# Kernel tuning notes

Hardware: AMD Instinct MI355X
Metric: run time of the kernel (lower is better)

## Reference

```python
import jax, jax.numpy as jnp
import numpy as np

# config constants
D = 1024       # main_dim
HD = 64        # attn_head_dim
NH = 16        # attention heads = D // HD
H = 16         # main_head_num (routing heads)
KH = 8         # main_key_head_num
KC = 2         # main_key_repeat_num (KH*KC == H)
N = 128        # block_size
E = 4096       # total_layer_expert_num
RE = 4         # aux_router_expert_num
DE = 4         # selected experts per router
ET = RE * DE   # 16
B, S = 1, 2048
T = B * S
BC = T // N    # 16
EPS = 1e-5
THETA = 10000.0


def rmsnorm(x, w):
    return x * jax.lax.rsqrt(jnp.mean(x * x, axis=-1, keepdims=True) + EPS) * w


def l2norm(x):
    n = jnp.sqrt(jnp.sum(x * x, axis=-1, keepdims=True))
    return x / jnp.maximum(n, EPS)


def rope(x):
    # x: (b, h, s, a); matches RotaryEmb: y1 = x1*cos + x2*sin, y2 = -x1*sin + x2*cos
    a = x.shape[-1]
    s = x.shape[2]
    inv_freq = (1.0 / THETA) ** (jnp.arange(0, a, 2, dtype=jnp.float32) / a)
    freqs = jnp.arange(s, dtype=jnp.float32)[:, None] * inv_freq[None, :]  # (s, a/2)
    cos, sin = jnp.cos(freqs), jnp.sin(freqs)
    x1, x2 = jnp.split(x, 2, axis=-1)
    return jnp.concatenate([x1 * cos + x2 * sin, -x1 * sin + x2 * cos], axis=-1)


def setup_inputs() -> dict:
    key = jax.random.key(0)
    ks = jax.random.split(key, 10)
    return {
        "x_input": jax.random.normal(ks[0], (B, S, D), jnp.float32),
        "indices": jax.random.randint(ks[1], (BC, RE, DE), 0, E),
        "scores": jax.random.normal(ks[2], (T, ET, H), jnp.float32),
        "attn_w": jax.random.normal(ks[3], (D, 3 * D), jnp.float32) * 0.02,
        "attn_out_w": jax.random.normal(ks[4], (D, D), jnp.float32) * 0.02,
        "attn_norm_w": jnp.ones((D,), jnp.float32),
        "ffn_norm_w": jnp.ones((D,), jnp.float32),
        "ffn_experts": jax.random.normal(ks[5], (3, E, D, 1), jnp.float32) * 0.02,
        "keys": jax.random.normal(ks[6], (KH, D, E), jnp.float32) * 0.02,
        "head_probs": jnp.full((1, RE, E, H), 1.0 / H, jnp.float32)
                      + 0.01 * jax.random.normal(ks[7], (1, RE, E, H), jnp.float32),
        "score_probs": jnp.full((2, 1, RE, E, H), 0.5, jnp.float32)
                       + 0.01 * jax.random.normal(ks[8], (2, 1, RE, E, H), jnp.float32),
    }


def reference(x_input, indices, scores, attn_w, attn_out_w, attn_norm_w,
              ffn_norm_w, ffn_experts, keys, head_probs, score_probs):
    # --- attention block ---
    x = rmsnorm(x_input, attn_norm_w)
    qkv = x @ attn_w                                   # (b, s, 3d)
    xq, xk, xv = jnp.split(qkv, 3, axis=-1)

    def heads(t):  # 'b s (h a) -> b h s a'
        return t.reshape(B, S, NH, HD).transpose(0, 2, 1, 3)

    xq, xk, xv = heads(xq), heads(xk), heads(xv)
    xq, xk = l2norm(xq), l2norm(xk)                    # qk_norm
    xq, xk = rope(xq), rope(xk)

    att = jnp.einsum('bhqa,bhka->bhqk', xq, xk) / np.sqrt(HD)
    causal = jnp.tril(jnp.ones((S, S), bool))
    att = jnp.where(causal, att, -jnp.inf)
    att = jax.nn.softmax(att, axis=-1)
    x_attn = jnp.einsum('bhqk,bhka->bhqa', att, xv)
    x_attn = x_attn.transpose(0, 2, 1, 3).reshape(B, S, D)
    x_attn_output = x_attn @ attn_out_w
    x_ffn_input = x_attn_output + x_input

    # --- product-key routing ---
    x_ffn = rmsnorm(x_ffn_input, ffn_norm_w)
    xf = x_ffn.reshape(T, D)

    keys_r = jnp.repeat(keys, KC, axis=0)              # (H, D, E)
    ms = jnp.einsum('td,hde->teh', xf, keys_r)         # (T, E, H)

    idx_flat = indices.reshape(BC, ET)                 # (BC, ET)
    idx_tok = jnp.repeat(idx_flat, N, axis=0)          # (T, ET), token t -> block t//N
    main_g = jnp.take_along_axis(ms, idx_tok[:, :, None], axis=1)  # (T, ET, H)

    r_idx = jnp.arange(RE)[None, :, None]
    sp = score_probs[:, 0]                             # (2, RE, E, H)
    sp_g = sp[:, r_idx, indices]                       # (2, BC, RE, DE, H)
    sp_g = jnp.repeat(sp_g.reshape(2, BC, ET, H), N, axis=1)       # (2, T, ET, H)

    comb = jax.nn.sigmoid(sp_g[0] * main_g + sp_g[1] * scores)     # (T, ET, H)

    hp_g = head_probs[0][r_idx, indices]               # (BC, RE, DE, H)
    hp_g = jnp.repeat(hp_g.reshape(BC, ET, H), N, axis=0)          # (T, ET, H)

    w = jnp.sum(comb * hp_g, axis=-1)                  # (T, ET) pair weights

    # --- grouped GEMM over tiny (d -> expert_dim -> d) experts, SwiGLU ---
    Wg = ffn_experts[:, idx_tok]                       # (3, T, ET, D, expert_dim)
    h0 = jnp.einsum('td,tedk->tek', xf, Wg[0])
    h1 = jnp.einsum('td,tedk->tek', xf, Wg[1])
    act = jax.nn.silu(h0) * h1 * w[:, :, None]         # (T, ET, expert_dim)
    out = jnp.einsum('tek,tedk->td', act, Wg[2])       # sum over selected experts

    return out.reshape(B, S, D) + x_ffn_input
```

## Files before the change

kernel.cpp:

```cpp
#include <hip/hip_runtime.h>
#include <hip/hip_bf16.h>
#include <math.h>

#define D_   1024
#define HD_  64
#define NH_  16
#define H_   16
#define KH_  8
#define NT_  128
#define E_   4096
#define RE_  4
#define DE_  4
#define ET_  16
#define S_   2048
#define T_   2048
#define BC_  16
#define EPS_ 1e-5f

typedef short s16x8 __attribute__((ext_vector_type(8)));
typedef float f32x4 __attribute__((ext_vector_type(4)));

__device__ __forceinline__ unsigned short f2bf(float f) {
    union { float f; unsigned int u; } v; v.f = f;
    unsigned int r = (v.u + 0x7fffu + ((v.u >> 16) & 1u)) >> 16;
    return (unsigned short)r;
}

#define GLOAD16(gp, lp) __builtin_amdgcn_global_load_lds(                      \
    (__attribute__((address_space(1))) void*)(gp),                             \
    (__attribute__((address_space(3))) void*)(lp), 16, 0, 0)

__global__ __launch_bounds__(256) void preprocess_kernel(
    const float* __restrict__ x, const float* __restrict__ attn_norm_w,
    unsigned short* __restrict__ xnb,
    const float* __restrict__ attn_w, unsigned short* __restrict__ wqkvT,
    const float* __restrict__ attn_out_w, unsigned short* __restrict__ woutT,
    const float* __restrict__ keys, const int* __restrict__ indices,
    unsigned short* __restrict__ kgath)
{
    __shared__ float tile[32][33];
    __shared__ float sred[4];
    int bid = blockIdx.x, tid = threadIdx.x;

    if (bid < 2048) {
        int row = bid;
        float4 v = ((const float4*)(x + (size_t)row * D_))[tid];
        float ss = v.x*v.x + v.y*v.y + v.z*v.z + v.w*v.w;
#pragma unroll
        for (int off = 32; off > 0; off >>= 1) ss += __shfl_xor(ss, off);
        if ((tid & 63) == 0) sred[tid >> 6] = ss;
        __syncthreads();
        float tot = sred[0] + sred[1] + sred[2] + sred[3];
        float scale = rsqrtf(tot * (1.0f / D_) + EPS_);
        float4 wv = ((const float4*)attn_norm_w)[tid];
        ushort4 o;
        o.x = f2bf(v.x * scale * wv.x);
        o.y = f2bf(v.y * scale * wv.y);
        o.z = f2bf(v.z * scale * wv.z);
        o.w = f2bf(v.w * scale * wv.w);
        *(ushort4*)(xnb + (size_t)row * D_ + tid * 4) = o;
    } else if (bid < 6144) {
        const float* src; unsigned short* dst; int R, Ncols, bx, by;
        if (bid < 5120) {
            int cid = bid - 2048;
            src = attn_w; dst = wqkvT; R = D_; Ncols = 3 * D_;
            bx = (cid % 96) * 32; by = (cid / 96) * 32;
        } else {
            int cid = bid - 5120;
            src = attn_out_w; dst = woutT; R = D_; Ncols = D_;
            bx = (cid & 31) * 32; by = (cid >> 5) * 32;
        }
        int tx = tid & 31, ty = tid >> 5;
#pragma unroll
        for (int rr = 0; rr < 32; rr += 8)
            tile[ty + rr][tx] = src[(size_t)(by + ty + rr) * Ncols + bx + tx];
        __syncthreads();
#pragma unroll
        for (int rr = 0; rr < 32; rr += 8)
            dst[(size_t)(bx + ty + rr) * R + by + tx] = f2bf(tile[tx][ty + rr]);
    } else {
        int gid = bid - 6144;
        int pair = gid >> 3, kh = gid & 7;
        int idx = indices[pair];
        const float* kp = keys + (size_t)kh * D_ * E_ + idx;
        int d = tid * 4;
        ushort4 o;
        o.x = f2bf(kp[(size_t)(d + 0) * E_]);
        o.y = f2bf(kp[(size_t)(d + 1) * E_]);
        o.z = f2bf(kp[(size_t)(d + 2) * E_]);
        o.w = f2bf(kp[(size_t)(d + 3) * E_]);
        *(ushort4*)(kgath + ((size_t)pair * KH_ + kh) * D_ + d) = o;
    }
}

__global__ __launch_bounds__(256) void rmsnorm_dual_kernel(
    const float* __restrict__ x, const float* __restrict__ w,
    float* __restrict__ out, unsigned short* __restrict__ outb)
{
    int row = blockIdx.x, tid = threadIdx.x;
    __shared__ float sred[4];
    float4 v = ((const float4*)(x + (size_t)row * D_))[tid];
    float ss = v.x*v.x + v.y*v.y + v.z*v.z + v.w*v.w;
#pragma unroll
    for (int off = 32; off > 0; off >>= 1) ss += __shfl_xor(ss, off);
    if ((tid & 63) == 0) sred[tid >> 6] = ss;
    __syncthreads();
    float tot = sred[0] + sred[1] + sred[2] + sred[3];
    float scale = rsqrtf(tot * (1.0f / D_) + EPS_);
    float4 wv = ((const float4*)w)[tid];
    float4 o;
    o.x = v.x * scale * wv.x;
    o.y = v.y * scale * wv.y;
    o.z = v.z * scale * wv.z;
    o.w = v.w * scale * wv.w;
    ((float4*)(out + (size_t)row * D_))[tid] = o;
    ushort4 ob;
    ob.x = f2bf(o.x); ob.y = f2bf(o.y); ob.z = f2bf(o.z); ob.w = f2bf(o.w);
    *(ushort4*)(outb + (size_t)row * D_ + tid * 4) = ob;
}

__global__ __launch_bounds__(256) void transpose_v_kernel(
    const unsigned short* __restrict__ src, unsigned short* __restrict__ dst)
{
    __shared__ unsigned short tile[32][34];
    int h  = blockIdx.z;
    int d0 = blockIdx.x * 32;
    int s0 = blockIdx.y * 32;
    int tx = threadIdx.x & 31, ty = threadIdx.x >> 5;
    const unsigned short* sp = src + ((size_t)h * S_ + s0) * HD_ + d0;
#pragma unroll
    for (int rr = 0; rr < 32; rr += 8)
        tile[ty + rr][tx] = sp[(size_t)(ty + rr) * HD_ + tx];
    __syncthreads();
    unsigned short* dp = dst + ((size_t)h * HD_ + d0) * S_ + s0;
#pragma unroll
    for (int rr = 0; rr < 32; rr += 8)
        dp[(size_t)(ty + rr) * S_ + tx] = tile[tx][ty + rr];
}

template <int WITH_RES>
__global__ __launch_bounds__(256) void mfma_gemm_kernel(
    const unsigned short* __restrict__ A, const unsigned short* __restrict__ Bt,
    const float* __restrict__ res, float* __restrict__ C,
    int M, int N, int K)
{
    __shared__ __align__(16) short As[128][32];
    __shared__ __align__(16) short Bs[128][32];
    int tid = threadIdx.x;
    int wave = tid >> 6, lane = tid & 63;
    int ml = lane & 15, q = lane >> 4;
    int wr = wave >> 1, wc = wave & 1;
    int bm = blockIdx.y * 128, bn = blockIdx.x * 128;
    int srow = tid >> 2;
    int scol = (tid & 3) * 8;

    f32x4 acc[4][4];
#pragma unroll
    for (int i = 0; i < 4; i++)
#pragma unroll
        for (int j = 0; j < 4; j++) acc[i][j] = (f32x4){0.f, 0.f, 0.f, 0.f};

    const unsigned short* Ap = A  + (size_t)(bm + srow) * K + scol;
    const unsigned short* Bp = Bt + (size_t)(bn + srow) * K + scol;
    short* ldsA0 = &As[wave * 16][0];
    short* ldsA1 = &As[64 + wave * 16][0];
    short* ldsB0 = &Bs[wave * 16][0];
    short* ldsB1 = &Bs[64 + wave * 16][0];

    for (int k0 = 0; k0 < K; k0 += 32) {
        __syncthreads();
        GLOAD16(Ap + k0, ldsA0);
        GLOAD16(Ap + (size_t)64 * K + k0, ldsA1);
        GLOAD16(Bp + k0, ldsB0);
        GLOAD16(Bp + (size_t)64 * K + k0, ldsB1);
        __syncthreads();

        s16x8 af[4], bf[4];
#pragma unroll
        for (int i = 0; i < 4; i++)
            af[i] = *(const s16x8*)(&As[wr * 64 + i * 16 + ml][q * 8]);
#pragma unroll
        for (int j = 0; j < 4; j++)
            bf[j] = *(const s16x8*)(&Bs[wc * 64 + j * 16 + ml][q * 8]);
#pragma unroll
        for (int i = 0; i < 4; i++)
#pragma unroll
            for (int j = 0; j < 4; j++)
                acc[i][j] = __builtin_amdgcn_mfma_f32_16x16x32_bf16(
                    af[i], bf[j], acc[i][j], 0, 0, 0);
    }

#pragma unroll
    for (int i = 0; i < 4; i++) {
#pragma unroll
        for (int j = 0; j < 4; j++) {
            int col = bn + wc * 64 + j * 16 + ml;
#pragma unroll
            for (int r = 0; r < 4; r++) {
                int row = bm + wr * 64 + i * 16 + q * 4 + r;
                float v = acc[i][j][r];
                if (WITH_RES) v += res[(size_t)row * N + col];
                C[(size_t)row * N + col] = v;
            }
        }
    }
}

__global__ __launch_bounds__(256) void mfma_gemm_qkv_kernel(
    const unsigned short* __restrict__ A, const unsigned short* __restrict__ Bt,
    unsigned short* __restrict__ qh, unsigned short* __restrict__ khb,
    unsigned short* __restrict__ vhb)
{
    const int K = D_;
    __shared__ __align__(16) short As[128][32];
    __shared__ __align__(16) short Bs[128][32];
    int tid = threadIdx.x;
    int wave = tid >> 6, lane = tid & 63;
    int ml = lane & 15, q = lane >> 4;
    int wr = wave >> 1, wc = wave & 1;
    int bm = blockIdx.y * 128, bn = blockIdx.x * 128;
    int srow = tid >> 2;
    int scol = (tid & 3) * 8;

    f32x4 acc[4][4];
#pragma unroll
    for (int i = 0; i < 4; i++)
#pragma unroll
        for (int j = 0; j < 4; j++) acc[i][j] = (f32x4){0.f, 0.f, 0.f, 0.f};

    const unsigned short* Ap = A  + (size_t)(bm + srow) * K + scol;
    const unsigned short* Bp = Bt + (size_t)(bn + srow) * K + scol;
    short* ldsA0 = &As[wave * 16][0];
    short* ldsA1 = &As[64 + wave * 16][0];
    short* ldsB0 = &Bs[wave * 16][0];
    short* ldsB1 = &Bs[64 + wave * 16][0];

    for (int k0 = 0; k0 < K; k0 += 32) {
        __syncthreads();
        GLOAD16(Ap + k0, ldsA0);
        GLOAD16(Ap + (size_t)64 * K + k0, ldsA1);
        GLOAD16(Bp + k0, ldsB0);
        GLOAD16(Bp + (size_t)64 * K + k0, ldsB1);
        __syncthreads();

        s16x8 af[4], bf[4];
#pragma unroll
        for (int i = 0; i < 4; i++)
            af[i] = *(const s16x8*)(&As[wr * 64 + i * 16 + ml][q * 8]);
#pragma unroll
        for (int j = 0; j < 4; j++)
            bf[j] = *(const s16x8*)(&Bs[wc * 64 + j * 16 + ml][q * 8]);
#pragma unroll
        for (int i = 0; i < 4; i++)
#pragma unroll
            for (int j = 0; j < 4; j++)
                acc[i][j] = __builtin_amdgcn_mfma_f32_16x16x32_bf16(
                    af[i], bf[j], acc[i][j], 0, 0, 0);
    }

    int sel = blockIdx.x >> 3;
    int h = ((blockIdx.x & 7) << 1) + wc;
    unsigned short* dst = (sel == 0) ? qh : (sel == 1) ? khb : vhb;
    float qscale = (sel == 0) ? 0.125f : 1.0f;
    float if0 = exp2f((float)ml * (-13.287712379549449f / 32.0f));
    float if1 = exp2f((float)(16 + ml) * (-13.287712379549449f / 32.0f));

#pragma unroll
    for (int i = 0; i < 4; i++) {
#pragma unroll
        for (int r = 0; r < 4; r++) {
            int row = bm + wr * 64 + i * 16 + q * 4 + r;
            float v0 = acc[i][0][r], v1 = acc[i][1][r];
            float v2 = acc[i][2][r], v3 = acc[i][3][r];
            if (sel < 2) {
                float ss = v0*v0 + v1*v1 + v2*v2 + v3*v3;
#pragma unroll
                for (int off = 1; off < 16; off <<= 1)
                    ss += __shfl_xor(ss, off);
                float inv = qscale / fmaxf(sqrtf(ss), EPS_);
                v0 *= inv; v1 *= inv; v2 *= inv; v3 *= inv;
                float sn0, cs0, sn1, cs1;
                sincosf((float)row * if0, &sn0, &cs0);
                sincosf((float)row * if1, &sn1, &cs1);
                float o0 = v0 * cs0 + v2 * sn0;
                float o2 = v2 * cs0 - v0 * sn0;
                float o1 = v1 * cs1 + v3 * sn1;
                float o3 = v3 * cs1 - v1 * sn1;
                v0 = o0; v1 = o1; v2 = o2; v3 = o3;
            }
            size_t base = ((size_t)h * S_ + row) * HD_;
            dst[base +      ml] = f2bf(v0);
            dst[base + 16 + ml] = f2bf(v1);
            dst[base + 32 + ml] = f2bf(v2);
            dst[base + 48 + ml] = f2bf(v3);
        }
    }
}

#define FS 72
__global__ __launch_bounds__(256) void flash_attn_mfma_kernel(
    const unsigned short* __restrict__ qh, const unsigned short* __restrict__ khb,
    const unsigned short* __restrict__ vhT, unsigned short* __restrict__ aob)
{
    __shared__ __align__(16) short Ks[2][64][FS];
    __shared__ __align__(16) short Vs[2][64][FS];
    __shared__ __align__(16) short Ps[4][16][FS];
    int b = blockIdx.x;
    int xcd = b & 7, j = b >> 3;
    int h = 2 * xcd + (j & 1);
    int pp = (j >> 1) & 15;
    int t = (j >> 5) ? (31 - pp) : pp;
    int tid = threadIdx.x;
    int wq = tid >> 6;
    int lane = tid & 63;
    int ml = lane & 15, quad = lane >> 4;
    int srow = tid >> 2;
    int sc = (tid & 3) * 16;
    const unsigned short* Qb = qh  + (size_t)h * S_ * HD_;
    const unsigned short* Kb = khb + (size_t)h * S_ * HD_;
    const unsigned short* Vt = vhT + (size_t)h * HD_ * S_;

    int q0 = t * 64;
    int qrow = q0 + wq * 16 + ml;
    s16x8 aq0 = *(const s16x8*)(Qb + (size_t)qrow * HD_ + quad * 8);
    s16x8 aq1 = *(const s16x8*)(Qb + (size_t)qrow * HD_ + 32 + quad * 8);

    float ps[4];
    f32x4 o[4];
#pragma unroll
    for (int r = 0; r < 4; r++) ps[r] = 0.f;
#pragma unroll
    for (int nb = 0; nb < 4; nb++) o[nb] = (f32x4){0.f, 0.f, 0.f, 0.f};

    int4 kr0, kr1, vr0, vr1;
    {
        const unsigned short* kp = Kb + (size_t)srow * HD_ + sc;
        kr0 = *(const int4*)kp; kr1 = *(const int4*)(kp + 8);
        const unsigned short* vp = Vt + (size_t)srow * S_ + sc;
        vr0 = *(const int4*)vp; vr1 = *(const int4*)(vp + 8);
        *(int4*)(&Ks[0][srow][sc]) = kr0; *(int4*)(&Ks[0][srow][sc + 8]) = kr1;
        *(int4*)(&Vs[0][srow][sc]) = vr0; *(int4*)(&Vs[0][srow][sc + 8]) = vr1;
    }

    for (int kt = 0; kt <= t; kt++) {
        int k0 = kt * 64;
        int cur = kt & 1;
        if (kt < t) {
            const unsigned short* kp = Kb + (size_t)(k0 + 64 + srow) * HD_ + sc;
            kr0 = *(const int4*)kp; kr1 = *(const int4*)(kp + 8);
            const unsigned short* vp = Vt + (size_t)srow * S_ + k0 + 64 + sc;
            vr0 = *(const int4*)vp; vr1 = *(const int4*)(vp + 8);
        }
        __syncthreads();

        f32x4 s[4];
#pragma unroll
        for (int nb = 0; nb < 4; nb++) s[nb] = (f32x4){0.f, 0.f, 0.f, 0.f};
        __builtin_amdgcn_s_setprio(1);
#pragma unroll
        for (int nb = 0; nb < 4; nb++) {
            s16x8 b0 = *(const s16x8*)(&Ks[cur][nb * 16 + ml][quad * 8]);
            s16x8 b1 = *(const s16x8*)(&Ks[cur][nb * 16 + ml][32 + quad * 8]);
            s[nb] = __builtin_amdgcn_mfma_f32_16x16x32_bf16(aq0, b0, s[nb], 0, 0, 0);
            s[nb] = __builtin_amdgcn_mfma_f32_16x16x32_bf16(aq1, b1, s[nb], 0, 0, 0);
        }
        __builtin_amdgcn_s_setprio(0);

#pragma unroll
        for (int nb = 0; nb < 4; nb++)
#pragma unroll
            for (int r = 0; r < 4; r++) {
                float pe = __expf(s[nb][r]);
                if (kt == t && (nb * 16 + ml) > (wq * 16 + quad * 4 + r))
                    pe = 0.f;
                ps[r] += pe;
                Ps[wq][quad * 4 + r][nb * 16 + ml] = (short)f2bf(pe);
            }

        s16x8 ap0 = *(const s16x8*)(&Ps[wq][ml][quad * 8]);
        s16x8 ap1 = *(const s16x8*)(&Ps[wq][ml][32 + quad * 8]);
        __builtin_amdgcn_s_setprio(1);
#pragma unroll
        for (int nb = 0; nb < 4; nb++) {
            s16x8 b0 = *(const s16x8*)(&Vs[cur][nb * 16 + ml][quad * 8]);
            s16x8 b1 = *(const s16x8*)(&Vs[cur][nb * 16 + ml][32 + quad * 8]);
            o[nb] = __builtin_amdgcn_mfma_f32_16x16x32_bf16(ap0, b0, o[nb], 0, 0, 0);
            o[nb] = __builtin_amdgcn_mfma_f32_16x16x32_bf16(ap1, b1, o[nb], 0, 0, 0);
        }
        __builtin_amdgcn_s_setprio(0);

        if (kt < t) {
            *(int4*)(&Ks[cur ^ 1][srow][sc])     = kr0;
            *(int4*)(&Ks[cur ^ 1][srow][sc + 8]) = kr1;
            *(int4*)(&Vs[cur ^ 1][srow][sc])     = vr0;
            *(int4*)(&Vs[cur ^ 1][srow][sc + 8]) = vr1;
        }
    }

#pragma unroll
    for (int r = 0; r < 4; r++) {
        float l = ps[r];
#pragma unroll
        for (int off = 1; off < 16; off <<= 1)
            l += __shfl_xor(l, off);
        float inv = 1.0f / l;
        int row = q0 + wq * 16 + quad * 4 + r;
#pragma unroll
        for (int nb = 0; nb < 4; nb++)
            aob[(size_t)row * D_ + h * HD_ + nb * 16 + ml] =
                f2bf(o[nb][r] * inv);
    }
}

__global__ __launch_bounds__(256) void score_gemm_kernel(
    const unsigned short* __restrict__ xfb, const unsigned short* __restrict__ kgath,
    float* __restrict__ msbufp)
{
    __shared__ __align__(16) short As[128][32];
    __shared__ __align__(16) short Bs[128][32];
    int c  = blockIdx.x >> 3;
    int sk = blockIdx.x & 7;
    const unsigned short* A  = xfb   + (size_t)c * 128 * D_ + sk * 128;
    const unsigned short* Bt = kgath + (size_t)c * 128 * D_ + sk * 128;
    int tid = threadIdx.x;
    int wave = tid >> 6, lane = tid & 63;
    int ml = lane & 15, q = lane >> 4;
    int wr = wave >> 1, wc = wave & 1;
    int srow = tid >> 2;
    int scol = (tid & 3) * 8;

    f32x4 acc[4][4];
#pragma unroll
    for (int i = 0; i < 4; i++)
#pragma unroll
        for (int j = 0; j < 4; j++) acc[i][j] = (f32x4){0.f, 0.f, 0.f, 0.f};

    const unsigned short* Ap = A  + (size_t)srow * D_ + scol;
    const unsigned short* Bp = Bt + (size_t)srow * D_ + scol;
    short* ldsA0 = &As[wave * 16][0];
    short* ldsA1 = &As[64 + wave * 16][0];
    short* ldsB0 = &Bs[wave * 16][0];
    short* ldsB1 = &Bs[64 + wave * 16][0];

    for (int k0 = 0; k0 < 128; k0 += 32) {
        __syncthreads();
        GLOAD16(Ap + k0, ldsA0);
        GLOAD16(Ap + (size_t)64 * D_ + k0, ldsA1);
        GLOAD16(Bp + k0, ldsB0);
        GLOAD16(Bp + (size_t)64 * D_ + k0, ldsB1);
        __syncthreads();

        s16x8 af[4], bf[4];
#pragma unroll
        for (int i = 0; i < 4; i++)
            af[i] = *(const s16x8*)(&As[wr * 64 + i * 16 + ml][q * 8]);
#pragma unroll
        for (int j = 0; j < 4; j++)
            bf[j] = *(const s16x8*)(&Bs[wc * 64 + j * 16 + ml][q * 8]);
#pragma unroll
        for (int i = 0; i < 4; i++)
#pragma unroll
            for (int j = 0; j < 4; j++)
                acc[i][j] = __builtin_amdgcn_mfma_f32_16x16x32_bf16(
                    af[i], bf[j], acc[i][j], 0, 0, 0);
    }

    float* out = msbufp + (size_t)blockIdx.x * 128 * 128;
#pragma unroll
    for (int i = 0; i < 4; i++)
#pragma unroll
        for (int j = 0; j < 4; j++) {
            int col = wc * 64 + j * 16 + ml;
#pragma unroll
            for (int r = 0; r < 4; r++) {
                int row = wr * 64 + i * 16 + q * 4 + r;
                out[(size_t)row * 128 + col] = acc[i][j][r];
            }
        }
}

__global__ __launch_bounds__(256) void moe_kernel(
    const float* __restrict__ xf, const float* __restrict__ xfi,
    const int* __restrict__ indices, const float* __restrict__ msbufp,
    const float* __restrict__ scores,
    const float* __restrict__ score_probs, const float* __restrict__ head_probs,
    const float* __restrict__ experts, float* __restrict__ out)
{
    int g = blockIdx.x, tid = threadIdx.x;
    int c = g >> 5;
    int t0 = c * NT_ + (g & 31) * 4;
    __shared__ int sidx[ET_];
    __shared__ float sw[4][ET_];
    __shared__ float sact[4][ET_];
    __shared__ float sx[4][D_];
    if (tid < ET_) sidx[tid] = indices[c * ET_ + tid];
#pragma unroll
    for (int tt = 0; tt < 4; tt++)
        ((float4*)sx[tt])[tid] =
            ((const float4*)(xf + (size_t)(t0 + tt) * D_))[tid];
    {
        int e = tid >> 4, hh = tid & 15;
        int idxe = indices[c * ET_ + e];
        int rr = e >> 2;
        float sp0 = score_probs[((size_t)rr * E_ + idxe) * H_ + hh];
        float sp1 = score_probs[((size_t)(RE_ + rr) * E_ + idxe) * H_ + hh];
        float hp  = head_probs[((size_t)rr * E_ + idxe) * H_ + hh];
#pragma unroll
        for (int tt = 0; tt < 4; tt++) {
            int t = t0 + tt;
            int trow = t & 127;
            const float* mp = msbufp + ((size_t)(c * 8) * 128 + trow) * 128
                                     + e * 8 + (hh >> 1);
            float ms = 0.f;
#pragma unroll
            for (int sck = 0; sck < 8; sck++)
                ms += mp[(size_t)sck * 128 * 128];
            float scv = scores[(size_t)t * (ET_ * H_) + tid];
            float z = sp0 * ms + sp1 * scv;
            float term = hp / (1.0f + __expf(-z));
#pragma unroll
            for (int off = 1; off < 16; off <<= 1)
                term += __shfl_xor(term, off);
            if (hh == 0) sw[tt][e] = term;
        }
    }
    __syncthreads();

    int wv = tid >> 6, lane = tid & 63;
#pragma unroll
    for (int ee = 0; ee < 4; ee++) {
        int e = wv * 4 + ee;
        int idx = sidx[e];
        size_t base = (size_t)idx * D_;
        float p0[4] = {0.f, 0.f, 0.f, 0.f};
        float p1[4] = {0.f, 0.f, 0.f, 0.f};
#pragma unroll
        for (int rr = 0; rr < 4; rr++) {
            int dd = rr * 256 + lane * 4;
            float4 w0 = *(const float4*)(experts + base + dd);
            float4 w1 = *(const float4*)(experts + (size_t)E_ * D_ + base + dd);
#pragma unroll
            for (int tt = 0; tt < 4; tt++) {
                float4 xr = *(const float4*)(&sx[tt][dd]);
                p0[tt] += xr.x*w0.x + xr.y*w0.y + xr.z*w0.z + xr.w*w0.w;
                p1[tt] += xr.x*w1.x + xr.y*w1.y + xr.z*w1.z + xr.w*w1.w;
            }
        }
#pragma unroll
        for (int tt = 0; tt < 4; tt++) {
#pragma unroll
            for (int off = 32; off > 0; off >>= 1) {
                p0[tt] += __shfl_xor(p0[tt], off);
                p1[tt] += __shfl_xor(p1[tt], off);
            }
        }
        if (lane == 0) {
#pragma unroll
            for (int tt = 0; tt < 4; tt++)
                sact[tt][e] = p0[tt] / (1.0f + __expf(-p0[tt])) * p1[tt]
                              * sw[tt][e];
        }
    }
    __syncthreads();

    float4 a0 = {0,0,0,0}, a1 = {0,0,0,0}, a2 = {0,0,0,0}, a3 = {0,0,0,0};
    const float* w2base = experts + (size_t)2 * E_ * D_;
#pragma unroll
    for (int e = 0; e < ET_; e++) {
        float4 w2 = *(const float4*)(w2base + (size_t)sidx[e] * D_ + tid * 4);
        float c0 = sact[0][e], c1 = sact[1][e], c2 = sact[2][e], c3 = sact[3][e];
        a0.x += c0 * w2.x; a0.y += c0 * w2.y; a0.z += c0 * w2.z; a0.w += c0 * w2.w;
        a1.x += c1 * w2.x; a1.y += c1 * w2.y; a1.z += c1 * w2.z; a1.w += c1 * w2.w;
        a2.x += c2 * w2.x; a2.y += c2 * w2.y; a2.z += c2 * w2.z; a2.w += c2 * w2.w;
        a3.x += c3 * w2.x; a3.y += c3 * w2.y; a3.z += c3 * w2.z; a3.w += c3 * w2.w;
    }
#pragma unroll
    for (int tt = 0; tt < 4; tt++) {
        float4 av = (tt == 0) ? a0 : (tt == 1) ? a1 : (tt == 2) ? a2 : a3;
        size_t o = (size_t)(t0 + tt) * D_ + tid * 4;
        float4 rv = *(const float4*)(xfi + o);
        float4 ov;
        ov.x = av.x + rv.x;
        ov.y = av.y + rv.y;
        ov.z = av.z + rv.z;
        ov.w = av.w + rv.w;
        *(float4*)(out + o) = ov;
    }
}

extern "C" void kernel_launch(void* const* d_in, const int* in_sizes, int n_in,
                              void* d_out, int out_size, void* d_ws, size_t ws_size,
                              hipStream_t stream)
{
    (void)in_sizes; (void)n_in; (void)out_size; (void)ws_size;
    const float* x_input     = (const float*)d_in[0];
    const int*   indices     = (const int*)d_in[1];
    const float* scores      = (const float*)d_in[2];
    const float* attn_w      = (const float*)d_in[3];
    const float* attn_out_w  = (const float*)d_in[4];
    const float* attn_norm_w = (const float*)d_in[5];
    const float* ffn_norm_w  = (const float*)d_in[6];
    const float* ffn_experts = (const float*)d_in[7];
    const float* keys        = (const float*)d_in[8];
    const float* head_probs  = (const float*)d_in[9];
    const float* score_probs = (const float*)d_in[10];
    float* out = (float*)d_out;

    float* ws = (float*)d_ws;
    const size_t MF = 1024 * 1024;
    unsigned short* qh    = (unsigned short*)ws;
    unsigned short* khb   = (unsigned short*)(ws + 1 * MF);
    unsigned short* vhb   = (unsigned short*)(ws + 2 * MF);
    unsigned short* vhT   = (unsigned short*)(ws + 3 * MF);
    float* xfi            = ws + 4 * MF;
    unsigned short* xnb   = (unsigned short*)(ws + 6 * MF);
    unsigned short* aob   = (unsigned short*)(ws + 6 * MF);
    unsigned short* woutT = (unsigned short*)(ws + 7 * MF);
    unsigned short* wqkvT = (unsigned short*)(ws + 8 * MF);
    float* xf             = ws + 8 * MF;
    unsigned short* kgath = (unsigned short*)(ws + 10 * MF);
    unsigned short* xfb   = (unsigned short*)(ws + 11 * MF);
    float* msbufp         = ws + 12 * MF;

    preprocess_kernel<<<8192, 256, 0, stream>>>(
        x_input, attn_norm_w, xnb, attn_w, wqkvT, attn_out_w, woutT,
        keys, indices, kgath);

    {
        dim3 g(3 * D_ / 128, T_ / 128);
        mfma_gemm_qkv_kernel<<<g, 256, 0, stream>>>(xnb, wqkvT, qh, khb, vhb);
    }

    {
        dim3 g(HD_ / 32, S_ / 32, NH_);
        transpose_v_kernel<<<g, 256, 0, stream>>>(vhb, vhT);
    }

    flash_attn_mfma_kernel<<<(S_ / 64) * NH_, 256, 0, stream>>>(qh, khb, vhT, aob);

    {
        dim3 g(D_ / 128, T_ / 128);
        mfma_gemm_kernel<1><<<g, 256, 0, stream>>>(aob, woutT, x_input, xfi,
                                                   T_, D_, D_);
    }

    rmsnorm_dual_kernel<<<T_, 256, 0, stream>>>(xfi, ffn_norm_w, xf, xfb);

    score_gemm_kernel<<<BC_ * 8, 256, 0, stream>>>(xfb, kgath, msbufp);

    moe_kernel<<<T_ / 4, 256, 0, stream>>>(xf, xfi, indices, msbufp, scores,
                                           score_probs, head_probs,
                                           ffn_experts, out);
}
```

Before: 375.0 us.

## Gather keys via coalesced row reads and fuse V transpose into QKV epilogue

The key-column gather, which did strided reads with stride E per element, is replaced by blocks that each load a full contiguous keys row into shared memory and pick the 256 selected columns. A new tiled transpose kernel then reorders the result into the kgath layout. Separately, the QKV GEMM epilogue now writes V directly in transposed layout, so the standalone V transpose kernel is removed. The trade-off is that the whole keys tensor is now streamed (128 MB of coalesced reads) and V is written with strided stores, in exchange for avoiding uncoalesced gathers and one kernel launch.

```diff
diff --git a/kernel.cpp b/kernel.cpp
--- a/kernel.cpp
+++ b/kernel.cpp
@@ -36,10 +36,11 @@
     const float* __restrict__ attn_w, unsigned short* __restrict__ wqkvT,
     const float* __restrict__ attn_out_w, unsigned short* __restrict__ woutT,
     const float* __restrict__ keys, const int* __restrict__ indices,
-    unsigned short* __restrict__ kgath)
+    unsigned short* __restrict__ tmpT)
 {
     __shared__ float tile[32][33];
     __shared__ float sred[4];
+    __shared__ float rowbuf[E_];
     int bid = blockIdx.x, tid = threadIdx.x;
 
     if (bid < 2048) {
@@ -79,17 +80,37 @@
         for (int rr = 0; rr < 32; rr += 8)
             dst[(size_t)(bx + ty + rr) * R + by + tx] = f2bf(tile[tx][ty + rr]);
     } else {
-        int gid = bid - 6144;
-        int pair = gid >> 3, kh = gid & 7;
-        int idx = indices[pair];
-        const float* kp = keys + (size_t)kh * D_ * E_ + idx;
-        int d = tid * 4;
-        ushort4 o;
-        o.x = f2bf(kp[(size_t)(d + 0) * E_]);
-        o.y = f2bf(kp[(size_t)(d + 1) * E_]);
-        o.z = f2bf(kp[(size_t)(d + 2) * E_]);
-        o.w = f2bf(kp[(size_t)(d + 3) * E_]);
-        *(ushort4*)(kgath + ((size_t)pair * KH_ + kh) * D_ + d) = o;
+        int id = bid - 6144;
+        int kh = id >> 10;
+        int d  = id & (D_ - 1);
+        const float* rowp = keys + ((size_t)kh * D_ + d) * E_;
+#pragma unroll
+        for (int pass = 0; pass < 4; pass++)
+            ((float4*)rowbuf)[tid + pass * 256] =
+                ((const float4*)rowp)[tid + pass * 256];
+        __syncthreads();
+        int idx = indices[tid];
+        tmpT[((size_t)kh * D_ + d) * 256 + tid] = f2bf(rowbuf[idx]);
+    }
+}
+
+__global__ __launch_bounds__(256) void transpose_keys_kernel(
+    const unsigned short* __restrict__ tmpT, unsigned short* __restrict__ kgath)
+{
+    __shared__ unsigned short tile[32][34];
+    int p0 = blockIdx.x * 32;
+    int d0 = blockIdx.y * 32;
+    int kh = blockIdx.z;
+    int tx = threadIdx.x & 31, ty = threadIdx.x >> 5;
+#pragma unroll
+    for (int rr = 0; rr < 32; rr += 8)
+        tile[ty + rr][tx] = tmpT[((size_t)kh * D_ + d0 + ty + rr) * 256 + p0 + tx];
+    __syncthreads();
+#pragma unroll
+    for (int rr = 0; rr < 32; rr += 8) {
+        int p = p0 + ty + rr;
+        int n = (p >> 4) * 128 + (p & 15) * 8 + kh;
+        kgath[(size_t)n * D_ + d0 + tx] = tile[tx][ty + rr];
     }
 }
 
@@ -119,25 +140,6 @@
     *(ushort4*)(outb + (size_t)row * D_ + tid * 4) = ob;
 }
 
-__global__ __launch_bounds__(256) void transpose_v_kernel(
-    const unsigned short* __restrict__ src, unsigned short* __restrict__ dst)
-{
-    __shared__ unsigned short tile[32][34];
-    int h  = blockIdx.z;
-    int d0 = blockIdx.x * 32;
-    int s0 = blockIdx.y * 32;
-    int tx = threadIdx.x & 31, ty = threadIdx.x >> 5;
-    const unsigned short* sp = src + ((size_t)h * S_ + s0) * HD_ + d0;
-#pragma unroll
-    for (int rr = 0; rr < 32; rr += 8)
-        tile[ty + rr][tx] = sp[(size_t)(ty + rr) * HD_ + tx];
-    __syncthreads();
-    unsigned short* dp = dst + ((size_t)h * HD_ + d0) * S_ + s0;
-#pragma unroll
-    for (int rr = 0; rr < 32; rr += 8)
-        dp[(size_t)(ty + rr) * S_ + tx] = tile[tx][ty + rr];
-}
-
 template <int WITH_RES>
 __global__ __launch_bounds__(256) void mfma_gemm_kernel(
     const unsigned short* __restrict__ A, const unsigned short* __restrict__ Bt,
@@ -209,7 +211,7 @@
 __global__ __launch_bounds__(256) void mfma_gemm_qkv_kernel(
     const unsigned short* __restrict__ A, const unsigned short* __restrict__ Bt,
     unsigned short* __restrict__ qh, unsigned short* __restrict__ khb,
-    unsigned short* __restrict__ vhb)
+    unsigned short* __restrict__ vhT)
 {
     const int K = D_;
     __shared__ __align__(16) short As[128][32];
@@ -260,7 +262,6 @@
 
     int sel = blockIdx.x >> 3;
     int h = ((blockIdx.x & 7) << 1) + wc;
-    unsigned short* dst = (sel == 0) ? qh : (sel == 1) ? khb : vhb;
     float qscale = (sel == 0) ? 0.125f : 1.0f;
     float if0 = exp2f((float)ml * (-13.287712379549449f / 32.0f));
     float if1 = exp2f((float)(16 + ml) * (-13.287712379549449f / 32.0f));
@@ -287,12 +288,19 @@
                 float o1 = v1 * cs1 + v3 * sn1;
                 float o3 = v3 * cs1 - v1 * sn1;
                 v0 = o0; v1 = o1; v2 = o2; v3 = o3;
+                unsigned short* dst = (sel == 0) ? qh : khb;
+                size_t base = ((size_t)h * S_ + row) * HD_;
+                dst[base +      ml] = f2bf(v0);
+                dst[base + 16 + ml] = f2bf(v1);
+                dst[base + 32 + ml] = f2bf(v2);
+                dst[base + 48 + ml] = f2bf(v3);
+            } else {
+                size_t base = ((size_t)h * HD_ + ml) * S_ + row;
+                vhT[base            ] = f2bf(v0);
+                vhT[base + 16 * S_  ] = f2bf(v1);
+                vhT[base + 32 * S_  ] = f2bf(v2);
+                vhT[base + 48 * S_  ] = f2bf(v3);
             }
-            size_t base = ((size_t)h * S_ + row) * HD_;
-            dst[base +      ml] = f2bf(v0);
-            dst[base + 16 + ml] = f2bf(v1);
-            dst[base + 32 + ml] = f2bf(v2);
-            dst[base + 48 + ml] = f2bf(v3);
         }
     }
 }
@@ -610,7 +618,7 @@
     const size_t MF = 1024 * 1024;
     unsigned short* qh    = (unsigned short*)ws;
     unsigned short* khb   = (unsigned short*)(ws + 1 * MF);
-    unsigned short* vhb   = (unsigned short*)(ws + 2 * MF);
+    unsigned short* tmpT  = (unsigned short*)(ws + 2 * MF);
     unsigned short* vhT   = (unsigned short*)(ws + 3 * MF);
     float* xfi            = ws + 4 * MF;
     unsigned short* xnb   = (unsigned short*)(ws + 6 * MF);
@@ -622,18 +630,18 @@
     unsigned short* xfb   = (unsigned short*)(ws + 11 * MF);
     float* msbufp         = ws + 12 * MF;
 
-    preprocess_kernel<<<8192, 256, 0, stream>>>(
+    preprocess_kernel<<<14336, 256, 0, stream>>>(
         x_input, attn_norm_w, xnb, attn_w, wqkvT, attn_out_w, woutT,
-        keys, indices, kgath);
+        keys, indices, tmpT);
+
+    {
+        dim3 g(256 / 32, D_ / 32, KH_);
+        transpose_keys_kernel<<<g, 256, 0, stream>>>(tmpT, kgath);
+    }
 
     {
         dim3 g(3 * D_ / 128, T_ / 128);
-        mfma_gemm_qkv_kernel<<<g, 256, 0, stream>>>(xnb, wqkvT, qh, khb, vhb);
-    }
-
-    {
-        dim3 g(HD_ / 32, S_ / 32, NH_);
-        transpose_v_kernel<<<g, 256, 0, stream>>>(vhb, vhT);
+        mfma_gemm_qkv_kernel<<<g, 256, 0, stream>>>(xnb, wqkvT, qh, khb, vhT);
     }
 
     flash_attn_mfma_kernel<<<(S_ / 64) * NH_, 256, 0, stream>>>(qh, khb, vhT, aob);
```

Result: no change. 372.4 us (-0.7%).
